# Optimization experiments

Hardware: AMD Instinct MI355X
Metric: run time of the kernel (lower is better)

Reference implementation:

```python
import jax, jax.numpy as jnp
import numpy as np

SMALL = -1000.0

def _crf_loss(pred, transitions, tags, seq_len):
    B, T, L = pred.shape
    START, STOP = L - 2, L - 1
    # pred[:, :, -2] = pred[:, :, -1] = small
    pred = pred.at[:, :, START].set(SMALL).at[:, :, STOP].set(SMALL)
    # start / end padding states
    start_state = jnp.full((B, 1, L), SMALL, pred.dtype).at[:, :, START].set(0.0)
    end_state = jnp.zeros((B, 1, L), pred.dtype)
    padded = jnp.concatenate([start_state, pred, end_state], axis=1)  # [B, T+2, L]
    b_idx = jnp.arange(B)
    padded = padded.at[b_idx, seq_len + 1, :].set(SMALL)
    padded = padded.at[b_idx, seq_len + 1, STOP].set(0.0)
    padded_t = jnp.transpose(padded, (1, 0, 2))  # [T+2, B, L]

    def step(prev, emit):
        # prev: [B, L] (from-label), emit: [B, L] (to-label)
        new = jax.nn.logsumexp(prev[:, :, None] + transitions[None, :, :] + emit[:, None, :], axis=1)
        return new, new

    _, alphas = jax.lax.scan(step, padded_t[0], padded_t[1:])  # [T+1, B, L]
    gathered = alphas[seq_len, b_idx, :]  # [B, L] (alphas at position seq_len)
    pred_paths_scores = jnp.sum(jax.nn.logsumexp(gathered, axis=1))

    # real path emission score
    pos = jnp.arange(T)
    mask = (pos[None, :] < seq_len[:, None]).astype(pred.dtype)  # [B, T]
    emit_score = jnp.take_along_axis(pred, tags[:, :, None], axis=2)[:, :, 0]  # [B, T]
    real_path_score = jnp.sum(emit_score * mask)

    # real path transition score
    start_tag = jnp.full((B, 1), START, tags.dtype)
    end_tag = jnp.zeros((B, 1), tags.dtype)
    padded_tags = jnp.concatenate([start_tag, tags, end_tag], axis=1)  # [B, T+2]
    padded_tags = padded_tags.at[b_idx, seq_len + 1].set(STOP)
    trans_score = transitions[padded_tags[:, :-1], padded_tags[:, 1:]]  # [B, T+1]
    tpos = jnp.arange(T + 1)
    tmask = (tpos[None, :] < (seq_len + 1)[:, None]).astype(pred.dtype)
    real_path_score = real_path_score + jnp.sum(trans_score * tmask)

    return pred_paths_scores - real_path_score


def setup_inputs() -> dict:
    key = jax.random.key(0)
    k1, k2, k3, k4 = jax.random.split(key, 4)
    B, T, L = 128, 1024, 128
    pred = jax.random.normal(k1, (B, T, L), dtype=jnp.float32)
    transitions = jax.random.normal(k2, (L, L), dtype=jnp.float32) * 0.1
    tags = jax.random.randint(k3, (B, T), 0, L - 2)  # real labels only, [0, L-3]
    seq_len = jax.random.randint(k4, (B,), 1, T + 1)
    return {"pred": pred, "transitions": transitions, "tags": tags, "seq_len": seq_len}


def reference(pred, transitions, tags, seq_len):
    return _crf_loss(pred, transitions, tags, seq_len)
```

## Files before the change

kernel.cpp:

```cpp
#include <hip/hip_runtime.h>

constexpr int L      = 128;
constexpr int TDIM   = 1024;
constexpr int NBATCH = 128;
constexpr int START  = L - 2;
constexpr int STOP   = L - 1;
constexpr int BSUB   = 16;
constexpr int NBLK   = NBATCH / BSUB;

typedef short bf16x8 __attribute__((ext_vector_type(8)));
typedef float f32x4  __attribute__((ext_vector_type(4)));
typedef int   i32x4  __attribute__((ext_vector_type(4)));

union B4 { i32x4 i; bf16x8 v; };

__device__ __forceinline__ short f2bf(float f) {
    unsigned x = __float_as_uint(f);
    return (short)((x + 0x7fffu + ((x >> 16) & 1u)) >> 16);
}
__device__ __forceinline__ unsigned pkbf(float lo, float hi) {
    unsigned r;
    asm("v_cvt_pk_bf16_f32 %0, %1, %2" : "=v"(r) : "v"(lo), "v"(hi));
    return r;
}

__global__ __launch_bounds__(256)
void crf_pexp(const float* __restrict__ pred, const int* __restrict__ seq_len,
              unsigned short* __restrict__ pexp)
{
    int gid  = blockIdx.x * 256 + threadIdx.x;
    int lane = gid & 63;
    int c    = (gid >> 6) & 3;
    int row  = (gid >> 8) & 1023;
    int blk  = gid >> 18;
    int l15 = lane & 15, l4 = lane >> 4;
    int b = blk * 16 + l15;
    bool live = row < seq_len[b];

    const float* src = pred + ((size_t)b * TDIM + row) * L + 32 * c + 4 * l4;
    f32x4 v0 = *(const f32x4*)(src);
    f32x4 v1 = *(const f32x4*)(src + 16);

    float e0[4], e1[4];
#pragma unroll
    for (int r = 0; r < 4; ++r) {
        int s0 = 32 * c + 4 * l4 + r;
        int s1 = s0 + 16;
        e0[r] = (live && s0 < 126) ? __expf(v0[r]) : 0.0f;
        e1[r] = (live && s1 < 126) ? __expf(v1[r]) : 0.0f;
    }
    i32x4 out;
    out[0] = (int)pkbf(e0[0], e0[1]);
    out[1] = (int)pkbf(e0[2], e0[3]);
    out[2] = (int)pkbf(e1[0], e1[1]);
    out[3] = (int)pkbf(e1[2], e1[3]);
    *(i32x4*)((char*)pexp + (size_t)gid * 16) = out;
}

struct PB { i32x4 c[4]; };
struct PF { f32x4 q[8]; };

__device__ __forceinline__ void pin_mfma_groups() {
    __builtin_amdgcn_sched_group_barrier(0x008, 8, 0);
    __builtin_amdgcn_sched_group_barrier(0x008, 8, 0);
    __builtin_amdgcn_sched_group_barrier(0x008, 8, 0);
    __builtin_amdgcn_sched_group_barrier(0x008, 8, 0);
}

template<bool PEXP>
__global__ __launch_bounds__(64, 1)
void crf_chain(const float* __restrict__ pred,
               const float* __restrict__ trans,
               const int* __restrict__ seq_len,
               const unsigned short* __restrict__ pexp,
               float* __restrict__ fwd_out)
{
    const int lane = threadIdx.x;
    const int l15 = lane & 15, l4 = lane >> 4;
    const int blk = blockIdx.x;
    const int b   = blk * BSUB + l15;

    bf16x8 A[8][4];
#pragma unroll
    for (int T = 0; T < 8; ++T)
#pragma unroll
        for (int kt = 0; kt < 4; ++kt) {
            bf16x8 v;
#pragma unroll
            for (int e = 0; e < 8; ++e) {
                int s = 16 * kt + 64 * (e >> 2) + 4 * l4 + (e & 3);
                v[e] = f2bf(__expf(trans[s * L + 16 * T + l15]));
            }
            A[T][kt] = v;
        }

    const int srow1 = seq_len[b] + 1;

    int mx = srow1;
#pragma unroll
    for (int d = 1; d < 16; d <<= 1) mx = max(mx, __shfl_xor(mx, d));
    const int tmaxR = __builtin_amdgcn_readfirstlane((mx + 1) & ~1);

    B4 B[4];
#pragma unroll
    for (int kt = 0; kt < 4; ++kt) B[kt].i = (i32x4){0, 0, 0, 0};
    if (l4 == 3) B[3].i[3] = 0x3F80;

    const f32x4 Z4 = {0.f, 0.f, 0.f, 0.f};

    float C = 0.0f;
    bool  applyScale = false;
    float res = 1.0f, resC = 0.0f;

    const char*  pxb = (const char*)pexp + (size_t)blk * 1024 * 4096;
    const float* pfb = pred + (size_t)b * TDIM * L + 4 * l4;

    auto loadPB = [&](PB& p, int row) {
        const i32x4* s = (const i32x4*)(pxb + (size_t)row * 4096) + lane;
        p.c[0] = s[0]; p.c[1] = s[64]; p.c[2] = s[128]; p.c[3] = s[192];
    };
    auto loadPF = [&](PF& p, int row) {
        const f32x4* s = (const f32x4*)(pfb + (size_t)row * L);
#pragma unroll
        for (int T = 0; T < 8; ++T) p.q[T] = s[T * 4];
    };

    auto stepP = [&](int t, PB& pb, bool chk) {
        f32x4 acc[8];
#pragma unroll
        for (int T = 0; T < 8; ++T)
            acc[T] = __builtin_amdgcn_mfma_f32_16x16x32_bf16(A[T][0], B[0].v, Z4, 0, 0, 0);
#pragma unroll
        for (int kt = 1; kt < 4; ++kt)
#pragma unroll
            for (int T = 0; T < 8; ++T)
                acc[T] = __builtin_amdgcn_mfma_f32_16x16x32_bf16(A[T][kt], B[kt].v, acc[T], 0, 0, 0);
        pin_mfma_groups();

        bool hit = (t == srow1);
        res  = hit ? acc[7][3] : res;
        resC = hit ? C : resC;

        float u[8][4];
#pragma unroll
        for (int T = 0; T < 8; ++T) {
            int cI = T >> 1, h = (T & 1) * 2;
            unsigned w0 = (unsigned)pb.c[cI][h + 0];
            unsigned w1 = (unsigned)pb.c[cI][h + 1];
            u[T][0] = acc[T][0] * __uint_as_float(w0 << 16);
            u[T][1] = acc[T][1] * __uint_as_float(w0 & 0xffff0000u);
            u[T][2] = acc[T][2] * __uint_as_float(w1 << 16);
            u[T][3] = acc[T][3] * __uint_as_float(w1 & 0xffff0000u);
        }
        if (applyScale) {
#pragma unroll
            for (int T = 0; T < 8; ++T)
#pragma unroll
                for (int r = 0; r < 4; ++r) u[T][r] *= 0x1p-64f;
            C += 44.3614195558365f;
        }
        applyScale = false;
        if (chk) {
            float m[8];
#pragma unroll
            for (int T = 0; T < 8; ++T)
                m[T] = fmaxf(fmaxf(u[T][0], u[T][1]), fmaxf(u[T][2], u[T][3]));
            float mx4 = fmaxf(fmaxf(fmaxf(m[0], m[1]), fmaxf(m[2], m[3])),
                              fmaxf(fmaxf(m[4], m[5]), fmaxf(m[6], m[7])));
            applyScale = (__ballot(mx4 > 0x1p80f) != 0ull);
        }

#pragma unroll
        for (int kt = 0; kt < 4; ++kt) {
            B[kt].i[0] = (int)pkbf(u[kt][0], u[kt][1]);
            B[kt].i[1] = (int)pkbf(u[kt][2], u[kt][3]);
            B[kt].i[2] = (int)pkbf(u[kt + 4][0], u[kt + 4][1]);
            B[kt].i[3] = (int)pkbf(u[kt + 4][2], u[kt + 4][3]);
        }
        loadPB(pb, min(t + 1, TDIM - 1));
    };

    auto stepF = [&](int t, PF& pf, bool chk) {
        f32x4 acc[8];
#pragma unroll
        for (int T = 0; T < 8; ++T)
            acc[T] = __builtin_amdgcn_mfma_f32_16x16x32_bf16(A[T][0], B[0].v, Z4, 0, 0, 0);
#pragma unroll
        for (int kt = 1; kt < 4; ++kt)
#pragma unroll
            for (int T = 0; T < 8; ++T)
                acc[T] = __builtin_amdgcn_mfma_f32_16x16x32_bf16(A[T][kt], B[kt].v, acc[T], 0, 0, 0);
        pin_mfma_groups();

        bool hit = (t == srow1);
        res  = hit ? acc[7][3] : res;
        resC = hit ? C : resC;

        const bool live = (t < srow1);
        float u[8][4];
#pragma unroll
        for (int T = 0; T < 8; ++T)
#pragma unroll
            for (int r = 0; r < 4; ++r) {
                bool dead = !live || (T == 7 && l4 == 3 && r >= 2);
                u[T][r] = dead ? 0.0f : acc[T][r] * __expf(pf.q[T][r]);
            }
        if (applyScale) {
#pragma unroll
            for (int T = 0; T < 8; ++T)
#pragma unroll
                for (int r = 0; r < 4; ++r) u[T][r] *= 0x1p-64f;
            C += 44.3614195558365f;
        }
        applyScale = false;
        if (chk) {
            float m[8];
#pragma unroll
            for (int T = 0; T < 8; ++T)
                m[T] = fmaxf(fmaxf(u[T][0], u[T][1]), fmaxf(u[T][2], u[T][3]));
            float mx4 = fmaxf(fmaxf(fmaxf(m[0], m[1]), fmaxf(m[2], m[3])),
                              fmaxf(fmaxf(m[4], m[5]), fmaxf(m[6], m[7])));
            applyScale = (__ballot(mx4 > 0x1p80f) != 0ull);
        }
#pragma unroll
        for (int kt = 0; kt < 4; ++kt) {
            B[kt].i[0] = (int)pkbf(u[kt][0], u[kt][1]);
            B[kt].i[1] = (int)pkbf(u[kt][2], u[kt][3]);
            B[kt].i[2] = (int)pkbf(u[kt + 4][0], u[kt + 4][1]);
            B[kt].i[3] = (int)pkbf(u[kt + 4][2], u[kt + 4][3]);
        }
        loadPF(pf, min(t + 1, TDIM - 1));
    };

    if constexpr (PEXP) {
        PB pa, pb_;
        loadPB(pa, 0); loadPB(pb_, 1);
        for (int t0 = 0; t0 < tmaxR; t0 += 2) {
            stepP(t0 + 1, pa, true);
            stepP(t0 + 2, pb_, false);
        }
    } else {
        PF fa, fb;
        loadPF(fa, 0); loadPF(fb, 1);
        for (int t0 = 0; t0 < tmaxR; t0 += 2) {
            stepF(t0 + 1, fa, true);
            stepF(t0 + 2, fb, false);
        }
    }

    if (l4 == 3)
        fwd_out[b] = __logf(res) + resC;
}

__global__ __launch_bounds__(256)
void crf_score(const float* __restrict__ pred,
               const float* __restrict__ trans,
               const int* __restrict__ tags,
               const int* __restrict__ seq_len,
               float* __restrict__ score_out)
{
    const int b = blockIdx.x;
    const int tid = threadIdx.x;
    const int sl = seq_len[b];
    const int* tg = tags + b * TDIM;

    float s = 0.0f;
    for (int t = tid; t < sl; t += 256) {
        int tag = tg[t];
        s += pred[((long)b * TDIM + t) * L + tag];
        int prev = (t == 0) ? START : tg[t - 1];
        s += trans[prev * L + tag];
    }
    if (tid == 0) s += trans[tg[sl - 1] * L + STOP];

    __shared__ float red[4];
#pragma unroll
    for (int d = 1; d < 64; d <<= 1) s += __shfl_xor(s, d);
    if ((tid & 63) == 0) red[tid >> 6] = s;
    __syncthreads();
    if (tid == 0) score_out[b] = (red[0] + red[1]) + (red[2] + red[3]);
}

__global__ __launch_bounds__(128)
void crf_combine(const float* __restrict__ fwd,
                 const float* __restrict__ real,
                 float* __restrict__ out)
{
    const int tid = threadIdx.x;
    float s = fwd[tid] - real[tid];
#pragma unroll
    for (int d = 1; d < 64; d <<= 1) s += __shfl_xor(s, d);
    __shared__ float red[2];
    if ((tid & 63) == 0) red[tid >> 6] = s;
    __syncthreads();
    if (tid == 0) out[0] = red[0] + red[1];
}

extern "C" void kernel_launch(void* const* d_in, const int* in_sizes, int n_in,
                              void* d_out, int out_size, void* d_ws, size_t ws_size,
                              hipStream_t stream)
{
    const float* pred    = (const float*)d_in[0];
    const float* trans   = (const float*)d_in[1];
    const int*   tags    = (const int*)d_in[2];
    const int*   seq_len = (const int*)d_in[3];

    float* ws   = (float*)d_ws;
    float* fwd  = ws;
    float* real = ws + 128;

    const size_t pexp_bytes = (size_t)NBLK * 1024 * 4096;
    if (ws_size >= 1024 + pexp_bytes) {
        unsigned short* pexp = (unsigned short*)((char*)d_ws + 1024);
        crf_pexp<<<8192, 256, 0, stream>>>(pred, seq_len, pexp);
        crf_chain<true><<<NBLK, 64, 0, stream>>>(pred, trans, seq_len, pexp, fwd);
    } else {
        crf_chain<false><<<NBLK, 64, 0, stream>>>(pred, trans, seq_len, nullptr, fwd);
    }
    crf_score  <<<NBATCH, 256, 0, stream>>>(pred, trans, tags, seq_len, real);
    crf_combine<<<1, 128, 0, stream>>>(fwd, real, (float*)d_out);
}
```

Baseline: 481.3 us.

## Interleave elementwise scaling with MFMA groups in the serial CRF forward step

Restructures the precomputed-exp path of the CRF forward recurrence so the per-step elementwise multiply, bf16 pack and overflow check run in stages interleaved with the four k-slices of MFMAs. Each k-slice of the next step's B operand is produced just before the MFMA group that consumes it, and explicit sched_group_barrier hints pin the VALU/MFMA order. The aim is to hide VALU latency behind matrix-core work on the serial dependency chain. In exchange, the overflow-rescale bookkeeping moves to a different point in the step, and correctness depends on the macro ordering matching the accumulator ping-pong between the two buffers.

```diff
diff --git a/kernel.cpp b/kernel.cpp
--- a/kernel.cpp
+++ b/kernel.cpp
@@ -60,12 +60,67 @@
 struct PB { i32x4 c[4]; };
 struct PF { f32x4 q[8]; };
 
-__device__ __forceinline__ void pin_mfma_groups() {
-    __builtin_amdgcn_sched_group_barrier(0x008, 8, 0);
-    __builtin_amdgcn_sched_group_barrier(0x008, 8, 0);
-    __builtin_amdgcn_sched_group_barrier(0x008, 8, 0);
-    __builtin_amdgcn_sched_group_barrier(0x008, 8, 0);
-}
+#define STAGE(TA, TB, ACCIN, PBUF, CHK, SCL)                                 \
+  {                                                                          \
+    unsigned wa0 = (unsigned)PBUF.c[(TA) >> 1][((TA) & 1) * 2 + 0];          \
+    unsigned wa1 = (unsigned)PBUF.c[(TA) >> 1][((TA) & 1) * 2 + 1];          \
+    unsigned wb0 = (unsigned)PBUF.c[(TB) >> 1][((TB) & 1) * 2 + 0];          \
+    unsigned wb1 = (unsigned)PBUF.c[(TB) >> 1][((TB) & 1) * 2 + 1];          \
+    float ua0 = ACCIN[TA][0] * __uint_as_float(wa0 << 16);                   \
+    float ua1 = ACCIN[TA][1] * __uint_as_float(wa0 & 0xffff0000u);           \
+    float ua2 = ACCIN[TA][2] * __uint_as_float(wa1 << 16);                   \
+    float ua3 = ACCIN[TA][3] * __uint_as_float(wa1 & 0xffff0000u);           \
+    float ub0 = ACCIN[TB][0] * __uint_as_float(wb0 << 16);                   \
+    float ub1 = ACCIN[TB][1] * __uint_as_float(wb0 & 0xffff0000u);           \
+    float ub2 = ACCIN[TB][2] * __uint_as_float(wb1 << 16);                   \
+    float ub3 = ACCIN[TB][3] * __uint_as_float(wb1 & 0xffff0000u);           \
+    if ((SCL) && applyScale) {                                               \
+      ua0 *= 0x1p-64f; ua1 *= 0x1p-64f; ua2 *= 0x1p-64f; ua3 *= 0x1p-64f;    \
+      ub0 *= 0x1p-64f; ub1 *= 0x1p-64f; ub2 *= 0x1p-64f; ub3 *= 0x1p-64f;    \
+    }                                                                        \
+    if (CHK) {                                                               \
+      mloc = fmaxf(mloc, fmaxf(fmaxf(fmaxf(ua0, ua1), fmaxf(ua2, ua3)),      \
+                               fmaxf(fmaxf(ub0, ub1), fmaxf(ub2, ub3))));    \
+    }                                                                        \
+    B[TA].i[0] = (int)pkbf(ua0, ua1);                                        \
+    B[TA].i[1] = (int)pkbf(ua2, ua3);                                        \
+    B[TA].i[2] = (int)pkbf(ub0, ub1);                                        \
+    B[TA].i[3] = (int)pkbf(ub2, ub3);                                        \
+    __builtin_amdgcn_sched_group_barrier(0x002, 20, 0);                      \
+  }
+
+#define GROUP(ACCO, KT, SEED)                                                \
+  {                                                                          \
+    ACCO[0] = __builtin_amdgcn_mfma_f32_16x16x32_bf16(A[0][KT], B[KT].v, (SEED) ? Z4 : ACCO[0], 0, 0, 0); \
+    ACCO[4] = __builtin_amdgcn_mfma_f32_16x16x32_bf16(A[4][KT], B[KT].v, (SEED) ? Z4 : ACCO[4], 0, 0, 0); \
+    ACCO[1] = __builtin_amdgcn_mfma_f32_16x16x32_bf16(A[1][KT], B[KT].v, (SEED) ? Z4 : ACCO[1], 0, 0, 0); \
+    ACCO[5] = __builtin_amdgcn_mfma_f32_16x16x32_bf16(A[5][KT], B[KT].v, (SEED) ? Z4 : ACCO[5], 0, 0, 0); \
+    ACCO[2] = __builtin_amdgcn_mfma_f32_16x16x32_bf16(A[2][KT], B[KT].v, (SEED) ? Z4 : ACCO[2], 0, 0, 0); \
+    ACCO[6] = __builtin_amdgcn_mfma_f32_16x16x32_bf16(A[6][KT], B[KT].v, (SEED) ? Z4 : ACCO[6], 0, 0, 0); \
+    ACCO[3] = __builtin_amdgcn_mfma_f32_16x16x32_bf16(A[3][KT], B[KT].v, (SEED) ? Z4 : ACCO[3], 0, 0, 0); \
+    ACCO[7] = __builtin_amdgcn_mfma_f32_16x16x32_bf16(A[7][KT], B[KT].v, (SEED) ? Z4 : ACCO[7], 0, 0, 0); \
+    __builtin_amdgcn_sched_group_barrier(0x008, 8, 0);                       \
+  }
+
+#define ITER(T_, ACCIN, ACCOUT, PBUF, CHK, SCL)                              \
+  {                                                                          \
+    const int tS = (T_);                                                     \
+    float mloc = 0.0f; (void)mloc;                                           \
+    STAGE(0, 4, ACCIN, PBUF, CHK, SCL)                                       \
+    STAGE(1, 5, ACCIN, PBUF, CHK, SCL)                                       \
+    GROUP(ACCOUT, 0, true)                                                   \
+    STAGE(2, 6, ACCIN, PBUF, CHK, SCL)                                       \
+    GROUP(ACCOUT, 1, false)                                                  \
+    STAGE(3, 7, ACCIN, PBUF, CHK, SCL)                                       \
+    { bool hit = (tS == srow1);                                              \
+      res  = hit ? ACCIN[7][3] : res;                                        \
+      resC = hit ? C : resC; }                                               \
+    if ((SCL) && applyScale) { C += 44.3614195558365f; applyScale = false; } \
+    GROUP(ACCOUT, 2, false)                                                  \
+    GROUP(ACCOUT, 3, false)                                                  \
+    if (CHK) applyScale = (__ballot(mloc > 0x1p80f) != 0ull);                \
+    loadPB(PBUF, min(tS + 1, TDIM - 1));                                     \
+  }
 
 template<bool PEXP>
 __global__ __launch_bounds__(64, 1)
@@ -125,123 +180,73 @@
         for (int T = 0; T < 8; ++T) p.q[T] = s[T * 4];
     };
 
-    auto stepP = [&](int t, PB& pb, bool chk) {
-        f32x4 acc[8];
-#pragma unroll
-        for (int T = 0; T < 8; ++T)
-            acc[T] = __builtin_amdgcn_mfma_f32_16x16x32_bf16(A[T][0], B[0].v, Z4, 0, 0, 0);
-#pragma unroll
-        for (int kt = 1; kt < 4; ++kt)
-#pragma unroll
-            for (int T = 0; T < 8; ++T)
-                acc[T] = __builtin_amdgcn_mfma_f32_16x16x32_bf16(A[T][kt], B[kt].v, acc[T], 0, 0, 0);
-        pin_mfma_groups();
-
-        bool hit = (t == srow1);
-        res  = hit ? acc[7][3] : res;
-        resC = hit ? C : resC;
-
-        float u[8][4];
-#pragma unroll
-        for (int T = 0; T < 8; ++T) {
-            int cI = T >> 1, h = (T & 1) * 2;
-            unsigned w0 = (unsigned)pb.c[cI][h + 0];
-            unsigned w1 = (unsigned)pb.c[cI][h + 1];
-            u[T][0] = acc[T][0] * __uint_as_float(w0 << 16);
-            u[T][1] = acc[T][1] * __uint_as_float(w0 & 0xffff0000u);
-            u[T][2] = acc[T][2] * __uint_as_float(w1 << 16);
-            u[T][3] = acc[T][3] * __uint_as_float(w1 & 0xffff0000u);
-        }
-        if (applyScale) {
-#pragma unroll
-            for (int T = 0; T < 8; ++T)
-#pragma unroll
-                for (int r = 0; r < 4; ++r) u[T][r] *= 0x1p-64f;
-            C += 44.3614195558365f;
-        }
-        applyScale = false;
-        if (chk) {
-            float m[8];
-#pragma unroll
-            for (int T = 0; T < 8; ++T)
-                m[T] = fmaxf(fmaxf(u[T][0], u[T][1]), fmaxf(u[T][2], u[T][3]));
-            float mx4 = fmaxf(fmaxf(fmaxf(m[0], m[1]), fmaxf(m[2], m[3])),
-                              fmaxf(fmaxf(m[4], m[5]), fmaxf(m[6], m[7])));
-            applyScale = (__ballot(mx4 > 0x1p80f) != 0ull);
-        }
-
-#pragma unroll
-        for (int kt = 0; kt < 4; ++kt) {
-            B[kt].i[0] = (int)pkbf(u[kt][0], u[kt][1]);
-            B[kt].i[1] = (int)pkbf(u[kt][2], u[kt][3]);
-            B[kt].i[2] = (int)pkbf(u[kt + 4][0], u[kt + 4][1]);
-            B[kt].i[3] = (int)pkbf(u[kt + 4][2], u[kt + 4][3]);
-        }
-        loadPB(pb, min(t + 1, TDIM - 1));
-    };
-
-    auto stepF = [&](int t, PF& pf, bool chk) {
-        f32x4 acc[8];
-#pragma unroll
-        for (int T = 0; T < 8; ++T)
-            acc[T] = __builtin_amdgcn_mfma_f32_16x16x32_bf16(A[T][0], B[0].v, Z4, 0, 0, 0);
-#pragma unroll
-        for (int kt = 1; kt < 4; ++kt)
-#pragma unroll
-            for (int T = 0; T < 8; ++T)
-                acc[T] = __builtin_amdgcn_mfma_f32_16x16x32_bf16(A[T][kt], B[kt].v, acc[T], 0, 0, 0);
-        pin_mfma_groups();
-
-        bool hit = (t == srow1);
-        res  = hit ? acc[7][3] : res;
-        resC = hit ? C : resC;
-
-        const bool live = (t < srow1);
-        float u[8][4];
-#pragma unroll
-        for (int T = 0; T < 8; ++T)
-#pragma unroll
-            for (int r = 0; r < 4; ++r) {
-                bool dead = !live || (T == 7 && l4 == 3 && r >= 2);
-                u[T][r] = dead ? 0.0f : acc[T][r] * __expf(pf.q[T][r]);
-            }
-        if (applyScale) {
-#pragma unroll
-            for (int T = 0; T < 8; ++T)
-#pragma unroll
-                for (int r = 0; r < 4; ++r) u[T][r] *= 0x1p-64f;
-            C += 44.3614195558365f;
-        }
-        applyScale = false;
-        if (chk) {
-            float m[8];
-#pragma unroll
-            for (int T = 0; T < 8; ++T)
-                m[T] = fmaxf(fmaxf(u[T][0], u[T][1]), fmaxf(u[T][2], u[T][3]));
-            float mx4 = fmaxf(fmaxf(fmaxf(m[0], m[1]), fmaxf(m[2], m[3])),
-                              fmaxf(fmaxf(m[4], m[5]), fmaxf(m[6], m[7])));
-            applyScale = (__ballot(mx4 > 0x1p80f) != 0ull);
-        }
-#pragma unroll
-        for (int kt = 0; kt < 4; ++kt) {
-            B[kt].i[0] = (int)pkbf(u[kt][0], u[kt][1]);
-            B[kt].i[1] = (int)pkbf(u[kt][2], u[kt][3]);
-            B[kt].i[2] = (int)pkbf(u[kt + 4][0], u[kt + 4][1]);
-            B[kt].i[3] = (int)pkbf(u[kt + 4][2], u[kt + 4][3]);
-        }
-        loadPF(pf, min(t + 1, TDIM - 1));
-    };
-
     if constexpr (PEXP) {
         PB pa, pb_;
         loadPB(pa, 0); loadPB(pb_, 1);
-        for (int t0 = 0; t0 < tmaxR; t0 += 2) {
-            stepP(t0 + 1, pa, true);
-            stepP(t0 + 2, pb_, false);
+
+        f32x4 accX[8], accY[8];
+        GROUP(accX, 0, true)
+        GROUP(accX, 1, false)
+        GROUP(accX, 2, false)
+        GROUP(accX, 3, false)
+
+        for (int t0 = 1; t0 < tmaxR; t0 += 2) {
+            ITER(t0,     accX, accY, pa,  true,  false)
+            ITER(t0 + 1, accY, accX, pb_, false, true)
         }
     } else {
         PF fa, fb;
         loadPF(fa, 0); loadPF(fb, 1);
+        f32x4 acc[8];
+        auto stepF = [&](int t, PF& pf, bool chk) {
+#pragma unroll
+            for (int T = 0; T < 8; ++T)
+                acc[T] = __builtin_amdgcn_mfma_f32_16x16x32_bf16(A[T][0], B[0].v, Z4, 0, 0, 0);
+#pragma unroll
+            for (int kt = 1; kt < 4; ++kt)
+#pragma unroll
+                for (int T = 0; T < 8; ++T)
+                    acc[T] = __builtin_amdgcn_mfma_f32_16x16x32_bf16(A[T][kt], B[kt].v, acc[T], 0, 0, 0);
+
+            bool hit = (t == srow1);
+            res  = hit ? acc[7][3] : res;
+            resC = hit ? C : resC;
+
+            const bool live = (t < srow1);
+            float u[8][4];
+#pragma unroll
+            for (int T = 0; T < 8; ++T)
+#pragma unroll
+                for (int r = 0; r < 4; ++r) {
+                    bool dead = !live || (T == 7 && l4 == 3 && r >= 2);
+                    u[T][r] = dead ? 0.0f : acc[T][r] * __expf(pf.q[T][r]);
+                }
+            if (applyScale) {
+#pragma unroll
+                for (int T = 0; T < 8; ++T)
+#pragma unroll
+                    for (int r = 0; r < 4; ++r) u[T][r] *= 0x1p-64f;
+                C += 44.3614195558365f;
+            }
+            applyScale = false;
+            if (chk) {
+                float m[8];
+#pragma unroll
+                for (int T = 0; T < 8; ++T)
+                    m[T] = fmaxf(fmaxf(u[T][0], u[T][1]), fmaxf(u[T][2], u[T][3]));
+                float mx4 = fmaxf(fmaxf(fmaxf(m[0], m[1]), fmaxf(m[2], m[3])),
+                                  fmaxf(fmaxf(m[4], m[5]), fmaxf(m[6], m[7])));
+                applyScale = (__ballot(mx4 > 0x1p80f) != 0ull);
+            }
+#pragma unroll
+            for (int kt = 0; kt < 4; ++kt) {
+                B[kt].i[0] = (int)pkbf(u[kt][0], u[kt][1]);
+                B[kt].i[1] = (int)pkbf(u[kt][2], u[kt][3]);
+                B[kt].i[2] = (int)pkbf(u[kt + 4][0], u[kt + 4][1]);
+                B[kt].i[3] = (int)pkbf(u[kt + 4][2], u[kt + 4][3]);
+            }
+            loadPF(pf, min(t + 1, TDIM - 1));
+        };
         for (int t0 = 0; t0 < tmaxR; t0 += 2) {
             stepF(t0 + 1, fa, true);
             stepF(t0 + 2, fb, false);
```

Result: no change. 480.5 us (median of 2 runs) (-0.2%).

## Split forward chain MFMA work across two waves with LDS exchange

Applied to the files above, without the earlier changes.

Replaces the single-wave forward recursion with a two-wave block in which each wave computes half of the output labels (four of the eight 16-row tiles). The halves of the next-step B operand are exchanged through double-buffered LDS with a __syncthreads per step, and the overflow-rescale trigger is shared between the waves. The aim is to halve the serial MFMA and elementwise latency on the critical path of the recurrence. In exchange, every step now pays a barrier plus LDS round trip, and the sched_group_barrier pinning is removed.

```diff
diff --git a/kernel.cpp b/kernel.cpp
--- a/kernel.cpp
+++ b/kernel.cpp
@@ -57,23 +57,170 @@
     *(i32x4*)((char*)pexp + (size_t)gid * 16) = out;
 }
 
-struct PB { i32x4 c[4]; };
-struct PF { f32x4 q[8]; };
-
-__device__ __forceinline__ void pin_mfma_groups() {
-    __builtin_amdgcn_sched_group_barrier(0x008, 8, 0);
-    __builtin_amdgcn_sched_group_barrier(0x008, 8, 0);
-    __builtin_amdgcn_sched_group_barrier(0x008, 8, 0);
-    __builtin_amdgcn_sched_group_barrier(0x008, 8, 0);
-}
-
-template<bool PEXP>
+struct PH { i32x4 q[2]; };
+
+__global__ __launch_bounds__(128, 1)
+void crf_chain_split(const float* __restrict__ pred,
+                     const float* __restrict__ trans,
+                     const int* __restrict__ seq_len,
+                     const unsigned short* __restrict__ pexp,
+                     float* __restrict__ fwd_out)
+{
+    const int tid  = threadIdx.x;
+    const int lane = tid & 63;
+    const int w    = tid >> 6;
+    const int l15 = lane & 15, l4 = lane >> 4;
+    const int blk = blockIdx.x;
+    const int b   = blk * BSUB + l15;
+
+    __shared__ int lds[2 * 16 * 64 + 4];
+
+    bf16x8 A4[4][4];
+#pragma unroll
+    for (int Tl = 0; Tl < 4; ++Tl)
+#pragma unroll
+        for (int kt = 0; kt < 4; ++kt) {
+            bf16x8 v;
+#pragma unroll
+            for (int e = 0; e < 8; ++e) {
+                int s = 16 * kt + 64 * (e >> 2) + 4 * l4 + (e & 3);
+                v[e] = f2bf(__expf(trans[s * L + 16 * (4 * w + Tl) + l15]));
+            }
+            A4[Tl][kt] = v;
+        }
+
+    const int srow1 = seq_len[b] + 1;
+    int mx = srow1;
+#pragma unroll
+    for (int d = 1; d < 16; d <<= 1) mx = max(mx, __shfl_xor(mx, d));
+    const int tmaxR = __builtin_amdgcn_readfirstlane((mx + 1) & ~1);
+
+    const f32x4 Z4 = {0.f, 0.f, 0.f, 0.f};
+
+    B4 B[4];
+#pragma unroll
+    for (int kt = 0; kt < 4; ++kt) B[kt].i = (i32x4){0, 0, 0, 0};
+    if (w == 1 && l4 == 3) B[3].i[3] = 0x3F80;
+
+    float C = 0.0f;
+    bool  applyScale = false;
+    float res = 1.0f, resC = 0.0f;
+
+    const char* pxb = (const char*)pexp + ((size_t)blk << 22) + (size_t)w * 2048;
+    auto loadPH = [&](PH& p, int row) {
+        const char* s = pxb + (size_t)row * 4096 + (size_t)lane * 16;
+        p.q[0] = *(const i32x4*)s;
+        p.q[1] = *(const i32x4*)(s + 1024);
+    };
+    PH pa, pb_;
+    loadPH(pa, 0); loadPH(pb_, 1);
+
+    f32x4 acc[4];
+
+    auto EXCH = [&](int par, int tS, bool CHK, bool myTrig) {
+        int* base = lds + par * 1024 + lane;
+        if (w == 0) {
+#pragma unroll
+            for (int kt = 0; kt < 4; ++kt) {
+                base[(2 * kt + 0) * 64] = B[kt].i[0];
+                base[(2 * kt + 1) * 64] = B[kt].i[1];
+            }
+        } else {
+#pragma unroll
+            for (int kt = 0; kt < 4; ++kt) {
+                base[(8 + 2 * kt + 0) * 64] = B[kt].i[2];
+                base[(8 + 2 * kt + 1) * 64] = B[kt].i[3];
+            }
+        }
+        if (CHK && lane == 0 && myTrig) lds[2048 + par * 2 + w] = tS;
+        __syncthreads();
+        if (w == 0) {
+#pragma unroll
+            for (int kt = 0; kt < 4; ++kt) {
+                B[kt].i[2] = base[(8 + 2 * kt + 0) * 64];
+                B[kt].i[3] = base[(8 + 2 * kt + 1) * 64];
+            }
+        } else {
+#pragma unroll
+            for (int kt = 0; kt < 4; ++kt) {
+                B[kt].i[0] = base[(2 * kt + 0) * 64];
+                B[kt].i[1] = base[(2 * kt + 1) * 64];
+            }
+        }
+        if (CHK) {
+            int of = lds[2048 + par * 2 + (1 - w)];
+            applyScale = myTrig || (of == tS);
+        }
+#pragma unroll
+        for (int Tl = 0; Tl < 4; ++Tl)
+            acc[Tl] = __builtin_amdgcn_mfma_f32_16x16x32_bf16(A4[Tl][0], B[0].v, Z4, 0, 0, 0);
+#pragma unroll
+        for (int kt = 1; kt < 4; ++kt)
+#pragma unroll
+            for (int Tl = 0; Tl < 4; ++Tl)
+                acc[Tl] = __builtin_amdgcn_mfma_f32_16x16x32_bf16(A4[Tl][kt], B[kt].v, acc[Tl], 0, 0, 0);
+    };
+
+    auto ITER = [&](int tS, PH& P, bool CHK, bool SCL) {
+        bool hit = (tS == srow1);
+        res  = hit ? acc[3][3] : res;
+        resC = hit ? C : resC;
+
+        float mloc = 0.0f;
+        unsigned Wd[4][2];
+#pragma unroll
+        for (int Tl = 0; Tl < 4; ++Tl) {
+            unsigned wa = (unsigned)P.q[Tl >> 1][(Tl & 1) * 2 + 0];
+            unsigned wb = (unsigned)P.q[Tl >> 1][(Tl & 1) * 2 + 1];
+            float u0 = acc[Tl][0] * __uint_as_float(wa << 16);
+            float u1 = acc[Tl][1] * __uint_as_float(wa & 0xffff0000u);
+            float u2 = acc[Tl][2] * __uint_as_float(wb << 16);
+            float u3 = acc[Tl][3] * __uint_as_float(wb & 0xffff0000u);
+            if (SCL && applyScale) {
+                u0 *= 0x1p-64f; u1 *= 0x1p-64f; u2 *= 0x1p-64f; u3 *= 0x1p-64f;
+            }
+            if (CHK)
+                mloc = fmaxf(mloc, fmaxf(fmaxf(u0, u1), fmaxf(u2, u3)));
+            Wd[Tl][0] = pkbf(u0, u1);
+            Wd[Tl][1] = pkbf(u2, u3);
+        }
+        if (SCL && applyScale) { C += 44.3614195558365f; applyScale = false; }
+
+        if (w == 0) {
+#pragma unroll
+            for (int kt = 0; kt < 4; ++kt) {
+                B[kt].i[0] = (int)Wd[kt][0];
+                B[kt].i[1] = (int)Wd[kt][1];
+            }
+        } else {
+#pragma unroll
+            for (int kt = 0; kt < 4; ++kt) {
+                B[kt].i[2] = (int)Wd[kt][0];
+                B[kt].i[3] = (int)Wd[kt][1];
+            }
+        }
+        bool myTrig = CHK ? (__ballot(mloc > 0x1p80f) != 0ull) : false;
+        EXCH(tS & 1, tS, CHK, myTrig);
+        loadPH(P, min(tS + 1, TDIM - 1));
+    };
+
+    if (tid < 4) lds[2048 + tid] = 0;
+    EXCH(0, 0, false, false);
+
+    for (int t0 = 1; t0 < tmaxR; t0 += 2) {
+        ITER(t0,     pa,  true,  false);
+        ITER(t0 + 1, pb_, false, true);
+    }
+
+    if (w == 1 && l4 == 3)
+        fwd_out[b] = __logf(res) + resC;
+}
+
 __global__ __launch_bounds__(64, 1)
-void crf_chain(const float* __restrict__ pred,
-               const float* __restrict__ trans,
-               const int* __restrict__ seq_len,
-               const unsigned short* __restrict__ pexp,
-               float* __restrict__ fwd_out)
+void crf_chain_fb(const float* __restrict__ pred,
+                  const float* __restrict__ trans,
+                  const int* __restrict__ seq_len,
+                  float* __restrict__ fwd_out)
 {
     const int lane = threadIdx.x;
     const int l15 = lane & 15, l4 = lane >> 4;
@@ -95,7 +242,6 @@
         }
 
     const int srow1 = seq_len[b] + 1;
-
     int mx = srow1;
 #pragma unroll
     for (int d = 1; d < 16; d <<= 1) mx = max(mx, __shfl_xor(mx, d));
@@ -107,26 +253,21 @@
     if (l4 == 3) B[3].i[3] = 0x3F80;
 
     const f32x4 Z4 = {0.f, 0.f, 0.f, 0.f};
-
     float C = 0.0f;
     bool  applyScale = false;
     float res = 1.0f, resC = 0.0f;
 
-    const char*  pxb = (const char*)pexp + (size_t)blk * 1024 * 4096;
     const float* pfb = pred + (size_t)b * TDIM * L + 4 * l4;
-
-    auto loadPB = [&](PB& p, int row) {
-        const i32x4* s = (const i32x4*)(pxb + (size_t)row * 4096) + lane;
-        p.c[0] = s[0]; p.c[1] = s[64]; p.c[2] = s[128]; p.c[3] = s[192];
-    };
+    struct PF { f32x4 q[8]; };
+    PF fa, fb;
     auto loadPF = [&](PF& p, int row) {
         const f32x4* s = (const f32x4*)(pfb + (size_t)row * L);
 #pragma unroll
         for (int T = 0; T < 8; ++T) p.q[T] = s[T * 4];
     };
-
-    auto stepP = [&](int t, PB& pb, bool chk) {
-        f32x4 acc[8];
+    loadPF(fa, 0); loadPF(fb, 1);
+    f32x4 acc[8];
+    auto stepF = [&](int t, PF& pf, bool chk) {
 #pragma unroll
         for (int T = 0; T < 8; ++T)
             acc[T] = __builtin_amdgcn_mfma_f32_16x16x32_bf16(A[T][0], B[0].v, Z4, 0, 0, 0);
@@ -135,23 +276,20 @@
 #pragma unroll
             for (int T = 0; T < 8; ++T)
                 acc[T] = __builtin_amdgcn_mfma_f32_16x16x32_bf16(A[T][kt], B[kt].v, acc[T], 0, 0, 0);
-        pin_mfma_groups();
 
         bool hit = (t == srow1);
         res  = hit ? acc[7][3] : res;
         resC = hit ? C : resC;
 
+        const bool live = (t < srow1);
         float u[8][4];
 #pragma unroll
-        for (int T = 0; T < 8; ++T) {
-            int cI = T >> 1, h = (T & 1) * 2;
-            unsigned w0 = (unsigned)pb.c[cI][h + 0];
-            unsigned w1 = (unsigned)pb.c[cI][h + 1];
-            u[T][0] = acc[T][0] * __uint_as_float(w0 << 16);
-            u[T][1] = acc[T][1] * __uint_as_float(w0 & 0xffff0000u);
-            u[T][2] = acc[T][2] * __uint_as_float(w1 << 16);
-            u[T][3] = acc[T][3] * __uint_as_float(w1 & 0xffff0000u);
-        }
+        for (int T = 0; T < 8; ++T)
+#pragma unroll
+            for (int r = 0; r < 4; ++r) {
+                bool dead = !live || (T == 7 && l4 == 3 && r >= 2);
+                u[T][r] = dead ? 0.0f : acc[T][r] * __expf(pf.q[T][r]);
+            }
         if (applyScale) {
 #pragma unroll
             for (int T = 0; T < 8; ++T)
@@ -169,7 +307,6 @@
                               fmaxf(fmaxf(m[4], m[5]), fmaxf(m[6], m[7])));
             applyScale = (__ballot(mx4 > 0x1p80f) != 0ull);
         }
-
 #pragma unroll
         for (int kt = 0; kt < 4; ++kt) {
             B[kt].i[0] = (int)pkbf(u[kt][0], u[kt][1]);
@@ -177,77 +314,12 @@
             B[kt].i[2] = (int)pkbf(u[kt + 4][0], u[kt + 4][1]);
             B[kt].i[3] = (int)pkbf(u[kt + 4][2], u[kt + 4][3]);
         }
-        loadPB(pb, min(t + 1, TDIM - 1));
-    };
-
-    auto stepF = [&](int t, PF& pf, bool chk) {
-        f32x4 acc[8];
-#pragma unroll
-        for (int T = 0; T < 8; ++T)
-            acc[T] = __builtin_amdgcn_mfma_f32_16x16x32_bf16(A[T][0], B[0].v, Z4, 0, 0, 0);
-#pragma unroll
-        for (int kt = 1; kt < 4; ++kt)
-#pragma unroll
-            for (int T = 0; T < 8; ++T)
-                acc[T] = __builtin_amdgcn_mfma_f32_16x16x32_bf16(A[T][kt], B[kt].v, acc[T], 0, 0, 0);
-        pin_mfma_groups();
-
-        bool hit = (t == srow1);
-        res  = hit ? acc[7][3] : res;
-        resC = hit ? C : resC;
-
-        const bool live = (t < srow1);
-        float u[8][4];
-#pragma unroll
-        for (int T = 0; T < 8; ++T)
-#pragma unroll
-            for (int r = 0; r < 4; ++r) {
-                bool dead = !live || (T == 7 && l4 == 3 && r >= 2);
-                u[T][r] = dead ? 0.0f : acc[T][r] * __expf(pf.q[T][r]);
-            }
-        if (applyScale) {
-#pragma unroll
-            for (int T = 0; T < 8; ++T)
-#pragma unroll
-                for (int r = 0; r < 4; ++r) u[T][r] *= 0x1p-64f;
-            C += 44.3614195558365f;
-        }
-        applyScale = false;
-        if (chk) {
-            float m[8];
-#pragma unroll
-            for (int T = 0; T < 8; ++T)
-                m[T] = fmaxf(fmaxf(u[T][0], u[T][1]), fmaxf(u[T][2], u[T][3]));
-            float mx4 = fmaxf(fmaxf(fmaxf(m[0], m[1]), fmaxf(m[2], m[3])),
-                              fmaxf(fmaxf(m[4], m[5]), fmaxf(m[6], m[7])));
-            applyScale = (__ballot(mx4 > 0x1p80f) != 0ull);
-        }
-#pragma unroll
-        for (int kt = 0; kt < 4; ++kt) {
-            B[kt].i[0] = (int)pkbf(u[kt][0], u[kt][1]);
-            B[kt].i[1] = (int)pkbf(u[kt][2], u[kt][3]);
-            B[kt].i[2] = (int)pkbf(u[kt + 4][0], u[kt + 4][1]);
-            B[kt].i[3] = (int)pkbf(u[kt + 4][2], u[kt + 4][3]);
-        }
         loadPF(pf, min(t + 1, TDIM - 1));
     };
-
-    if constexpr (PEXP) {
-        PB pa, pb_;
-        loadPB(pa, 0); loadPB(pb_, 1);
-        for (int t0 = 0; t0 < tmaxR; t0 += 2) {
-            stepP(t0 + 1, pa, true);
-            stepP(t0 + 2, pb_, false);
-        }
-    } else {
-        PF fa, fb;
-        loadPF(fa, 0); loadPF(fb, 1);
-        for (int t0 = 0; t0 < tmaxR; t0 += 2) {
-            stepF(t0 + 1, fa, true);
-            stepF(t0 + 2, fb, false);
-        }
-    }
-
+    for (int t0 = 0; t0 < tmaxR; t0 += 2) {
+        stepF(t0 + 1, fa, true);
+        stepF(t0 + 2, fb, false);
+    }
     if (l4 == 3)
         fwd_out[b] = __logf(res) + resC;
 }
@@ -309,13 +381,15 @@
     float* fwd  = ws;
     float* real = ws + 128;
 
-    const size_t pexp_bytes = (size_t)NBLK * 1024 * 4096;
-    if (ws_size >= 1024 + pexp_bytes) {
-        unsigned short* pexp = (unsigned short*)((char*)d_ws + 1024);
-        crf_pexp<<<8192, 256, 0, stream>>>(pred, seq_len, pexp);
-        crf_chain<true><<<NBLK, 64, 0, stream>>>(pred, trans, seq_len, pexp, fwd);
+    const size_t bf16_bytes = (size_t)NBLK * 1024 * 4096;
+    void* pxbuf = (char*)d_ws + 1024;
+
+    if (ws_size >= 1024 + bf16_bytes) {
+        crf_pexp<<<8192, 256, 0, stream>>>(pred, seq_len, (unsigned short*)pxbuf);
+        crf_chain_split<<<NBLK, 128, 0, stream>>>(pred, trans, seq_len,
+                                                  (const unsigned short*)pxbuf, fwd);
     } else {
-        crf_chain<false><<<NBLK, 64, 0, stream>>>(pred, trans, seq_len, nullptr, fwd);
+        crf_chain_fb<<<NBLK, 64, 0, stream>>>(pred, trans, seq_len, fwd);
     }
     crf_score  <<<NBATCH, 256, 0, stream>>>(pred, trans, tags, seq_len, real);
     crf_combine<<<1, 128, 0, stream>>>(fwd, real, (float*)d_out);
```

Result: slower. 721.6 us (+49.9%).
